# Kernel tuning notes

Hardware: AMD Instinct MI355X
Metric: run time of the kernel (lower is better)

The kernel has to match this reference:

```python
import jax, jax.numpy as jnp
import numpy as np

HIDDEN = 2048
N_HEADS = 32
N_KV_HEADS = 8
HEAD_DIM = HIDDEN // N_HEADS  # 64
N_REP = N_HEADS // N_KV_HEADS  # 4
ROPE_THETA = 10000.0


def setup_inputs() -> dict:
    key = jax.random.key(0)
    ks = jax.random.split(key, 5)
    b, s = 2, 2048
    x = jax.random.normal(ks[0], (b, s, HIDDEN), dtype=jnp.float32)
    position_ids = jnp.arange(b * s, dtype=jnp.int32).reshape(b, s)
    sc = 1.0 / np.sqrt(HIDDEN)
    Wq = jax.random.normal(ks[1], (HIDDEN, HIDDEN), dtype=jnp.float32) * sc
    Wk = jax.random.normal(ks[2], (HIDDEN, N_KV_HEADS * HEAD_DIM), dtype=jnp.float32) * sc
    Wv = jax.random.normal(ks[3], (HIDDEN, N_KV_HEADS * HEAD_DIM), dtype=jnp.float32) * sc
    Wo = jax.random.normal(ks[4], (HIDDEN, HIDDEN), dtype=jnp.float32) * sc
    return {"input_ids": x, "Wq": Wq, "Wk": Wk, "Wv": Wv, "Wo": Wo,
            "position_ids": position_ids}


def _rope_cos_sin(position_ids, dtype):
    # inv_freq: [head_dim/2]
    inv_freq = 1.0 / (ROPE_THETA ** (jnp.arange(0, HEAD_DIM, 2, dtype=jnp.float32) / HEAD_DIM))
    freqs = position_ids.astype(jnp.float32)[..., None] * inv_freq  # [b, s, d/2]
    emb = jnp.concatenate([freqs, freqs], axis=-1)  # [b, s, d]
    return emb.astype(dtype), None  # placeholder, replaced below


def _rotate_half(x):
    x1, x2 = jnp.split(x, 2, axis=-1)
    return jnp.concatenate([-x2, x1], axis=-1)


def reference(input_ids, Wq, Wk, Wv, Wo, position_ids):
    b, s, _ = input_ids.shape
    q = (input_ids @ Wq).reshape(b, s, N_HEADS, HEAD_DIM).transpose(0, 2, 1, 3)      # [b,H,s,d]
    k = (input_ids @ Wk).reshape(b, s, N_KV_HEADS, HEAD_DIM).transpose(0, 2, 1, 3)   # [b,Hkv,s,d]
    v = (input_ids @ Wv).reshape(b, s, N_KV_HEADS, HEAD_DIM).transpose(0, 2, 1, 3)

    # RoPE
    inv_freq = 1.0 / (ROPE_THETA ** (jnp.arange(0, HEAD_DIM, 2, dtype=jnp.float32) / HEAD_DIM))
    freqs = position_ids.astype(jnp.float32)[..., None] * inv_freq  # [b,s,d/2]
    emb = jnp.concatenate([freqs, freqs], axis=-1)                   # [b,s,d]
    cos = jnp.cos(emb).astype(input_ids.dtype)[:, None, :, :]        # [b,1,s,d]
    sin = jnp.sin(emb).astype(input_ids.dtype)[:, None, :, :]
    q = q * cos + _rotate_half(q) * sin
    k = k * cos + _rotate_half(k) * sin

    # repeat_kv: [b,Hkv,s,d] -> [b,H,s,d]
    k = jnp.repeat(k, N_REP, axis=1)
    v = jnp.repeat(v, N_REP, axis=1)

    # causal SDPA
    scale = 1.0 / np.sqrt(HEAD_DIM)
    scores = jnp.einsum('bhqd,bhkd->bhqk', q, k) * scale
    causal = jnp.tril(jnp.ones((s, s), dtype=bool))
    scores = jnp.where(causal, scores, jnp.finfo(scores.dtype).min)
    attn = jax.nn.softmax(scores, axis=-1)
    out = jnp.einsum('bhqk,bhkd->bhqd', attn, v)                     # [b,H,s,d]
    out = out.transpose(0, 2, 1, 3).reshape(b, s, HIDDEN)
    return out @ Wo
```

## Files before the change

kernel.cpp:

```cpp
#include <hip/hip_runtime.h>
#include <hip/hip_bf16.h>

#define HIDDEN 2048
#define NHEADS 32
#define NKVH   8
#define HD     64
#define BATCH  2
#define SEQ    2048
#define ROWS   (BATCH * SEQ)
#define NQKV   3072
#define KCOL   2048
#define VCOL   2560

typedef __bf16 bf16x8 __attribute__((ext_vector_type(8)));
typedef __bf16 bf16x4 __attribute__((ext_vector_type(4)));
typedef float  f32x4  __attribute__((ext_vector_type(4)));
typedef short  s16x4  __attribute__((ext_vector_type(4)));
typedef short  s16x8  __attribute__((ext_vector_type(8)));

__device__ __forceinline__ void gl2lds16(const void* g, void* l) {
  __builtin_amdgcn_global_load_lds(
      (const __attribute__((address_space(1))) void*)g,
      (__attribute__((address_space(3))) void*)l, 16, 0, 0);
}

__device__ __forceinline__ short f2bs(float f) {
  __bf16 h = (__bf16)f;
  return __builtin_bit_cast(short, h);
}

__device__ __forceinline__ float fexp2(float x) {
#if __has_builtin(__builtin_amdgcn_exp2f)
  return __builtin_amdgcn_exp2f(x);
#else
  return exp2f(x);
#endif
}

__device__ __forceinline__ f32x4 mfma16(s16x4 a, s16x4 b, f32x4 c) {
#if __has_builtin(__builtin_amdgcn_mfma_f32_16x16x16bf16_1k)
  return __builtin_amdgcn_mfma_f32_16x16x16bf16_1k(a, b, c, 0, 0, 0);
#else
  s16x8 a8 = __builtin_shufflevector(a, (s16x4){0,0,0,0}, 0,1,2,3,4,5,6,7);
  s16x8 b8 = __builtin_shufflevector(b, (s16x4){0,0,0,0}, 0,1,2,3,4,5,6,7);
  a8[4]=0;a8[5]=0;a8[6]=0;a8[7]=0; b8[4]=0;b8[5]=0;b8[6]=0;b8[7]=0;
  return __builtin_amdgcn_mfma_f32_16x16x32_bf16(
      __builtin_bit_cast(bf16x8, a8), __builtin_bit_cast(bf16x8, b8), c, 0, 0, 0);
#endif
}

__global__ void prep(const float* __restrict__ Wq, const float* __restrict__ Wk,
                     const float* __restrict__ Wv, const float* __restrict__ Wo,
                     const float* __restrict__ x,
                     __bf16* __restrict__ dstW, __bf16* __restrict__ Xb) {
  __shared__ __bf16 tile[32][33];
  int bid = blockIdx.x, tid = threadIdx.x;
  if (bid < 10240) {
    int n0 = (bid % 160) * 32, k0 = (bid / 160) * 32;
    int tx = tid & 31, ty = tid >> 5;
    const float* src;
    int N, c0;
    if (n0 < 2048)      { src = Wq; N = 2048; c0 = n0; }
    else if (n0 < 2560) { src = Wk; N = 512;  c0 = n0 - 2048; }
    else if (n0 < 3072) { src = Wv; N = 512;  c0 = n0 - 2560; }
    else                { src = Wo; N = 2048; c0 = n0 - 3072; }
#pragma unroll
    for (int i = 0; i < 32; i += 8)
      tile[ty + i][tx] = (__bf16)src[(size_t)(k0 + ty + i) * N + (c0 + tx)];
    __syncthreads();
#pragma unroll
    for (int i = 0; i < 32; i += 8)
      dstW[(size_t)(n0 + ty + i) * HIDDEN + (k0 + tx)] = tile[tx][ty + i];
  } else {
    size_t i = (size_t)(bid - 10240) * 256 + tid;
    const float4* s = (const float4*)(x + i * 16);
    float4 a = s[0], b = s[1], c = s[2], d = s[3];
    bf16x8 o0, o1;
    o0[0] = (__bf16)a.x; o0[1] = (__bf16)a.y; o0[2] = (__bf16)a.z; o0[3] = (__bf16)a.w;
    o0[4] = (__bf16)b.x; o0[5] = (__bf16)b.y; o0[6] = (__bf16)b.z; o0[7] = (__bf16)b.w;
    o1[0] = (__bf16)c.x; o1[1] = (__bf16)c.y; o1[2] = (__bf16)c.z; o1[3] = (__bf16)c.w;
    o1[4] = (__bf16)d.x; o1[5] = (__bf16)d.y; o1[6] = (__bf16)d.z; o1[7] = (__bf16)d.w;
    *(bf16x8*)(Xb + i * 16)     = o0;
    *(bf16x8*)(Xb + i * 16 + 8) = o1;
  }
}

template <typename OutT, bool ROPE>
__launch_bounds__(256, 2)
__global__ void gemm_bt(const __bf16* __restrict__ A, const __bf16* __restrict__ Bt,
                        OutT* __restrict__ C, int M, int N, int K,
                        const int* __restrict__ pos_ids, __bf16* __restrict__ Vt) {
  __shared__ __bf16 As[2][128 * 32];
  __shared__ __bf16 Bs[2][128 * 32];
  int id = blockIdx.x;
  int bm = (id & 7) * 4 + ((id >> 3) & 3);
  int bn = id >> 5;
  int t = threadIdx.x;
  int wave = t >> 6, lane = t & 63, l16 = lane & 15, quad = lane >> 4;
  int wm = (wave >> 1) * 64, wn = (wave & 1) * 64;

  f32x4 acc[4][4] = {};

  int arow = t >> 2;
  int ac   = (t & 3) * 8;
  const __bf16* Ag = A  + (size_t)(bm * 128 + arow) * K + ac;
  const __bf16* Bg = Bt + (size_t)(bn * 128 + arow) * K + ac;
  int woff = wave * 512;

  for (int k0 = 0; k0 < K; k0 += 64) {
    __syncthreads();
    gl2lds16(Ag + k0,                      &As[0][woff]);
    gl2lds16(Ag + (size_t)64 * K + k0,      &As[0][2048 + woff]);
    gl2lds16(Ag + k0 + 32,                 &As[1][woff]);
    gl2lds16(Ag + (size_t)64 * K + k0 + 32, &As[1][2048 + woff]);
    gl2lds16(Bg + k0,                      &Bs[0][woff]);
    gl2lds16(Bg + (size_t)64 * K + k0,      &Bs[0][2048 + woff]);
    gl2lds16(Bg + k0 + 32,                 &Bs[1][woff]);
    gl2lds16(Bg + (size_t)64 * K + k0 + 32, &Bs[1][2048 + woff]);
    __syncthreads();

#pragma unroll
    for (int ks = 0; ks < 2; ++ks) {
      bf16x8 af[4], bfr[4];
#pragma unroll
      for (int i = 0; i < 4; ++i) {
        af[i]  = *(const bf16x8*)(&As[ks][(wm + i * 16 + l16) * 32 + quad * 8]);
        bfr[i] = *(const bf16x8*)(&Bs[ks][(wn + i * 16 + l16) * 32 + quad * 8]);
      }
#pragma unroll
      for (int i = 0; i < 4; ++i)
#pragma unroll
        for (int j = 0; j < 4; ++j)
          acc[i][j] = __builtin_amdgcn_mfma_f32_16x16x32_bf16(af[i], bfr[j], acc[i][j], 0, 0, 0);
    }
  }

  if (ROPE) {
    int headidx = bn * 2 + (wn >> 6);
    if (headidx >= 40) {
#pragma unroll
      for (int i = 0; i < 4; ++i) {
        int srow = bm * 128 + wm + i * 16 + quad * 4;
        int b = srow >> 11, s = srow & 2047;
#pragma unroll
        for (int j = 0; j < 4; ++j) {
          int vcol = bn * 128 + wn + j * 16 + l16 - VCOL;
          int hk = vcol >> 6, d = vcol & 63;
          bf16x4 w;
#pragma unroll
          for (int r = 0; r < 4; ++r) w[r] = (__bf16)acc[i][j][r];
          *(bf16x4*)(Vt + ((size_t)(b * NKVH + hk) * HD + d) * SEQ + s) = w;
        }
      }
      return;
    }
    float invrev0 = __expf(-(float)l16 * 0.28782313662425574f) * 0.15915494309189535f;
    float invrev1 = __expf(-(float)(l16 + 16) * 0.28782313662425574f) * 0.15915494309189535f;
#pragma unroll
    for (int i = 0; i < 4; ++i)
#pragma unroll
      for (int r = 0; r < 4; ++r) {
        int gr = bm * 128 + wm + i * 16 + quad * 4 + r;
        float pos = (float)pos_ids[gr];
        float rv0 = pos * invrev0; rv0 -= floorf(rv0);
        float rv1 = pos * invrev1; rv1 -= floorf(rv1);
        float a0 = rv0 * 6.283185307179586f, a1 = rv1 * 6.283185307179586f;
        float s0 = __sinf(a0), c0 = __cosf(a0);
        float s1 = __sinf(a1), c1 = __cosf(a1);
        float x0 = acc[i][0][r], x2 = acc[i][2][r];
        acc[i][0][r] = x0 * c0 - x2 * s0;
        acc[i][2][r] = x2 * c0 + x0 * s0;
        float x1 = acc[i][1][r], x3 = acc[i][3][r];
        acc[i][1][r] = x1 * c1 - x3 * s1;
        acc[i][3][r] = x3 * c1 + x1 * s1;
      }
  }

#pragma unroll
  for (int i = 0; i < 4; ++i)
#pragma unroll
    for (int j = 0; j < 4; ++j)
#pragma unroll
      for (int r = 0; r < 4; ++r)
        C[(size_t)(bm * 128 + wm + i * 16 + quad * 4 + r) * N +
          (bn * 128 + wn + j * 16 + l16)] = (OutT)acc[i][j][r];
}

__launch_bounds__(256, 4)
__global__ void flash_attn(const __bf16* __restrict__ QKV, const __bf16* __restrict__ Vt,
                           __bf16* __restrict__ O) {
  int wgid = blockIdx.x + 64 * (blockIdx.y + 8 * (int)blockIdx.z);
  int swz  = (wgid & 7) * 128 + (wgid >> 3);
  int b  = swz >> 9;
  int hk = (swz >> 6) & 7;
  int bx = swz & 63;
  int p  = bx >> 2;
  int h  = hk * 4 + (bx & 3);

  int t = threadIdx.x;
  int wave = t >> 6, lane = t & 63, l16 = lane & 15, quad = lane >> 4;

  __shared__ __bf16 Ks[2][2][64 * 32];
  __shared__ __bf16 Vs[2][4096];

  const __bf16* Kbase = QKV + (size_t)(b * SEQ) * NQKV + KCOL + hk * HD;
  const __bf16* VtB   = Vt + (size_t)(b * NKVH + hk) * HD * SEQ;

  int kr = wave * 16 + (lane >> 2);
  int kc = (lane & 3) * 8;
  int vd = wave * 16 + (lane >> 2);
  int vsc = (lane & 3) * 16;
  int vs4w = (lane & 3) * 4;

  const s16x4 vones = { (short)0x3F80, (short)0x3F80, (short)0x3F80, (short)0x3F80 };

  for (int seg = 0; seg < 2; ++seg) {
    int qt = seg ? (31 - p) : p;

    __syncthreads();

    bf16x8 qfrag[2];
    {
      const __bf16* qp = QKV + (size_t)(b * SEQ + qt * 64 + wave * 16 + l16) * NQKV
                       + h * HD + quad * 8;
      bf16x8 q0 = *(const bf16x8*)qp;
      bf16x8 q1 = *(const bf16x8*)(qp + 32);
#pragma unroll
      for (int e = 0; e < 8; ++e) {
        qfrag[0][e] = (__bf16)((float)q0[e] * 0.18033688011112042f);
        qfrag[1][e] = (__bf16)((float)q1[e] * 0.18033688011112042f);
      }
    }

    f32x4 lacc = {0.f, 0.f, 0.f, 0.f};
    f32x4 oacc[4];
#pragma unroll
    for (int dt = 0; dt < 4; ++dt) oacc[dt] = (f32x4){0.f, 0.f, 0.f, 0.f};

    {
      const __bf16* kp = Kbase + (size_t)kr * NQKV + kc;
      gl2lds16(kp,      &Ks[0][0][wave * 512]);
      gl2lds16(kp + 32, &Ks[0][1][wave * 512]);
      const __bf16* vp = VtB + (size_t)vd * SEQ + vsc;
      s16x8 v0 = __builtin_bit_cast(s16x8, *(const bf16x8*)vp);
      s16x8 v1 = __builtin_bit_cast(s16x8, *(const bf16x8*)(vp + 8));
      *(s16x4*)(&Vs[0][(vs4w + 0) * 256 + vd * 4]) = __builtin_shufflevector(v0, v0, 0, 1, 2, 3);
      *(s16x4*)(&Vs[0][(vs4w + 1) * 256 + vd * 4]) = __builtin_shufflevector(v0, v0, 4, 5, 6, 7);
      *(s16x4*)(&Vs[0][(vs4w + 2) * 256 + vd * 4]) = __builtin_shufflevector(v1, v1, 0, 1, 2, 3);
      *(s16x4*)(&Vs[0][(vs4w + 3) * 256 + vd * 4]) = __builtin_shufflevector(v1, v1, 4, 5, 6, 7);
    }

    for (int kt = 0; kt <= qt; ++kt) {
      int buf = kt & 1;
      __syncthreads();

      bool pre = (kt < qt);
      s16x8 pv0, pv1;
      if (pre) {
        const __bf16* kp = Kbase + (size_t)((kt + 1) * 64 + kr) * NQKV + kc;
        gl2lds16(kp,      &Ks[buf ^ 1][0][wave * 512]);
        gl2lds16(kp + 32, &Ks[buf ^ 1][1][wave * 512]);
        const __bf16* vp = VtB + (size_t)vd * SEQ + (kt + 1) * 64 + vsc;
        pv0 = __builtin_bit_cast(s16x8, *(const bf16x8*)vp);
        pv1 = __builtin_bit_cast(s16x8, *(const bf16x8*)(vp + 8));
      }

      f32x4 sacc[4];
#pragma unroll
      for (int nt = 0; nt < 4; ++nt) sacc[nt] = (f32x4){0.f, 0.f, 0.f, 0.f};
#pragma unroll
      for (int ks = 0; ks < 2; ++ks) {
        bf16x8 kf[4];
#pragma unroll
        for (int nt = 0; nt < 4; ++nt)
          kf[nt] = *(const bf16x8*)(&Ks[buf][ks][(nt * 16 + l16) * 32 + quad * 8]);
#pragma unroll
        for (int nt = 0; nt < 4; ++nt)
          sacc[nt] = __builtin_amdgcn_mfma_f32_16x16x32_bf16(kf[nt], qfrag[ks], sacc[nt], 0, 0, 0);
      }

      s16x4 af[4];
      if (kt == qt) {
        int qg = wave * 16 + l16;
#pragma unroll
        for (int nt = 0; nt < 4; ++nt)
#pragma unroll
          for (int r = 0; r < 4; ++r) {
            int kg = nt * 16 + quad * 4 + r;
            float e = fexp2((kg > qg) ? -1e30f : sacc[nt][r]);
            af[nt][r] = f2bs(e);
          }
      } else {
#pragma unroll
        for (int nt = 0; nt < 4; ++nt)
#pragma unroll
          for (int r = 0; r < 4; ++r)
            af[nt][r] = f2bs(fexp2(sacc[nt][r]));
      }

#pragma unroll
      for (int nt = 0; nt < 4; ++nt) {
        s16x4 vf[4];
#pragma unroll
        for (int dt = 0; dt < 4; ++dt)
          vf[dt] = *(const s16x4*)(&Vs[buf][(nt * 4 + quad) * 256 + (dt * 16 + l16) * 4]);
#pragma unroll
        for (int dt = 0; dt < 4; ++dt)
          oacc[dt] = mfma16(af[nt], vf[dt], oacc[dt]);
        lacc = mfma16(af[nt], vones, lacc);
      }

      if (pre) {
        *(s16x4*)(&Vs[buf ^ 1][(vs4w + 0) * 256 + vd * 4]) = __builtin_shufflevector(pv0, pv0, 0, 1, 2, 3);
        *(s16x4*)(&Vs[buf ^ 1][(vs4w + 1) * 256 + vd * 4]) = __builtin_shufflevector(pv0, pv0, 4, 5, 6, 7);
        *(s16x4*)(&Vs[buf ^ 1][(vs4w + 2) * 256 + vd * 4]) = __builtin_shufflevector(pv1, pv1, 0, 1, 2, 3);
        *(s16x4*)(&Vs[buf ^ 1][(vs4w + 3) * 256 + vd * 4]) = __builtin_shufflevector(pv1, pv1, 4, 5, 6, 7);
      }
    }

#pragma unroll
    for (int r = 0; r < 4; ++r) {
      float inv = 1.0f / lacc[r];
#pragma unroll
      for (int dt = 0; dt < 4; ++dt) {
        float o = oacc[dt][r] * inv;
        O[(size_t)(b * SEQ + qt * 64 + wave * 16 + quad * 4 + r) * HIDDEN +
          h * HD + dt * 16 + l16] = (__bf16)o;
      }
    }
  }
}

extern "C" void kernel_launch(void* const* d_in, const int* in_sizes, int n_in,
                              void* d_out, int out_size, void* d_ws, size_t ws_size,
                              hipStream_t stream) {
  const float* x  = (const float*)d_in[0];
  const float* Wq = (const float*)d_in[1];
  const float* Wk = (const float*)d_in[2];
  const float* Wv = (const float*)d_in[3];
  const float* Wo = (const float*)d_in[4];
  const int* pos  = (const int*)d_in[5];

  __bf16* Wqkvt = (__bf16*)d_ws;
  __bf16* Wot   = Wqkvt + (size_t)NQKV * HIDDEN;
  __bf16* Xb    = Wot + (size_t)HIDDEN * HIDDEN;
  __bf16* QKV   = Xb + (size_t)ROWS * HIDDEN;
  __bf16* Oat   = QKV + (size_t)ROWS * NQKV;
  __bf16* Vt    = Xb;

  prep<<<dim3(12288), 256, 0, stream>>>(Wq, Wk, Wv, Wo, x, Wqkvt, Xb);

  gemm_bt<__bf16, true><<<dim3(768), 256, 0, stream>>>(
      Xb, Wqkvt, QKV, ROWS, NQKV, HIDDEN, pos, Vt);

  flash_attn<<<dim3(64, NKVH, BATCH), 256, 0, stream>>>(QKV, Vt, Oat);

  gemm_bt<float, false><<<dim3(512), 256, 0, stream>>>(
      Oat, Wot, (float*)d_out, ROWS, HIDDEN, HIDDEN, nullptr, nullptr);
}
```

Before: 276.8 us.

## Process both causal query tiles in one KV pass to share K/V loads

Each workgroup used to handle two query tiles (p and 31-p) one after another, streaming K/V from global memory separately for each. Now it holds both Q tiles in registers and makes a single pass over the KV tiles up to 31-p, applying each loaded K/V tile to both queries while kt <= p. This removes the duplicated K/V loads and barriers of the shorter pass, and s_setprio hints are added around the MFMA groups. The cost is more accumulator registers, which may lower occupancy under the 256x4 launch bounds, and divergent branch code for the a0 predicate.

After: 285.9 us. 3.3% more time.

```diff
diff --git a/kernel.cpp b/kernel.cpp
--- a/kernel.cpp
+++ b/kernel.cpp
@@ -195,6 +195,7 @@
   int hk = (swz >> 6) & 7;
   int bx = swz & 63;
   int p  = bx >> 2;
+  int np = 31 - p;
   int h  = hk * 4 + (bx & 3);
 
   int t = threadIdx.x;
@@ -214,116 +215,156 @@
 
   const s16x4 vones = { (short)0x3F80, (short)0x3F80, (short)0x3F80, (short)0x3F80 };
 
-  for (int seg = 0; seg < 2; ++seg) {
-    int qt = seg ? (31 - p) : p;
-
+  bf16x8 qfrag[2][2];
+#pragma unroll
+  for (int qi = 0; qi < 2; ++qi) {
+    int qt = qi ? np : p;
+    const __bf16* qp = QKV + (size_t)(b * SEQ + qt * 64 + wave * 16 + l16) * NQKV
+                     + h * HD + quad * 8;
+    bf16x8 q0 = *(const bf16x8*)qp;
+    bf16x8 q1 = *(const bf16x8*)(qp + 32);
+#pragma unroll
+    for (int e = 0; e < 8; ++e) {
+      qfrag[qi][0][e] = (__bf16)((float)q0[e] * 0.18033688011112042f);
+      qfrag[qi][1][e] = (__bf16)((float)q1[e] * 0.18033688011112042f);
+    }
+  }
+
+  f32x4 lacc[2] = { {0.f,0.f,0.f,0.f}, {0.f,0.f,0.f,0.f} };
+  f32x4 oacc[2][4];
+#pragma unroll
+  for (int qi = 0; qi < 2; ++qi)
+#pragma unroll
+    for (int dt = 0; dt < 4; ++dt) oacc[qi][dt] = (f32x4){0.f, 0.f, 0.f, 0.f};
+
+  {
+    const __bf16* kp = Kbase + (size_t)kr * NQKV + kc;
+    gl2lds16(kp,      &Ks[0][0][wave * 512]);
+    gl2lds16(kp + 32, &Ks[0][1][wave * 512]);
+    const __bf16* vp = VtB + (size_t)vd * SEQ + vsc;
+    s16x8 v0 = __builtin_bit_cast(s16x8, *(const bf16x8*)vp);
+    s16x8 v1 = __builtin_bit_cast(s16x8, *(const bf16x8*)(vp + 8));
+    *(s16x4*)(&Vs[0][(vs4w + 0) * 256 + vd * 4]) = __builtin_shufflevector(v0, v0, 0, 1, 2, 3);
+    *(s16x4*)(&Vs[0][(vs4w + 1) * 256 + vd * 4]) = __builtin_shufflevector(v0, v0, 4, 5, 6, 7);
+    *(s16x4*)(&Vs[0][(vs4w + 2) * 256 + vd * 4]) = __builtin_shufflevector(v1, v1, 0, 1, 2, 3);
+    *(s16x4*)(&Vs[0][(vs4w + 3) * 256 + vd * 4]) = __builtin_shufflevector(v1, v1, 4, 5, 6, 7);
+  }
+
+  for (int kt = 0; kt <= np; ++kt) {
+    int buf = kt & 1;
     __syncthreads();
 
-    bf16x8 qfrag[2];
+    bool pre = (kt < np);
+    s16x8 pv0, pv1;
+    if (pre) {
+      const __bf16* kp = Kbase + (size_t)((kt + 1) * 64 + kr) * NQKV + kc;
+      gl2lds16(kp,      &Ks[buf ^ 1][0][wave * 512]);
+      gl2lds16(kp + 32, &Ks[buf ^ 1][1][wave * 512]);
+      const __bf16* vp = VtB + (size_t)vd * SEQ + (kt + 1) * 64 + vsc;
+      pv0 = __builtin_bit_cast(s16x8, *(const bf16x8*)vp);
+      pv1 = __builtin_bit_cast(s16x8, *(const bf16x8*)(vp + 8));
+    }
+
+    bool a0 = (kt <= p);
+
+    f32x4 s0[4], s1[4];
+#pragma unroll
+    for (int nt = 0; nt < 4; ++nt) {
+      s0[nt] = (f32x4){0.f, 0.f, 0.f, 0.f};
+      s1[nt] = (f32x4){0.f, 0.f, 0.f, 0.f};
+    }
+#pragma unroll
+    for (int ks = 0; ks < 2; ++ks) {
+      bf16x8 kf[4];
+#pragma unroll
+      for (int nt = 0; nt < 4; ++nt)
+        kf[nt] = *(const bf16x8*)(&Ks[buf][ks][(nt * 16 + l16) * 32 + quad * 8]);
+      __builtin_amdgcn_s_setprio(1);
+#pragma unroll
+      for (int nt = 0; nt < 4; ++nt)
+        s1[nt] = __builtin_amdgcn_mfma_f32_16x16x32_bf16(kf[nt], qfrag[1][ks], s1[nt], 0, 0, 0);
+      if (a0) {
+#pragma unroll
+        for (int nt = 0; nt < 4; ++nt)
+          s0[nt] = __builtin_amdgcn_mfma_f32_16x16x32_bf16(kf[nt], qfrag[0][ks], s0[nt], 0, 0, 0);
+      }
+      __builtin_amdgcn_s_setprio(0);
+    }
+
+    s16x4 af0[4], af1[4];
     {
-      const __bf16* qp = QKV + (size_t)(b * SEQ + qt * 64 + wave * 16 + l16) * NQKV
-                       + h * HD + quad * 8;
-      bf16x8 q0 = *(const bf16x8*)qp;
-      bf16x8 q1 = *(const bf16x8*)(qp + 32);
-#pragma unroll
-      for (int e = 0; e < 8; ++e) {
-        qfrag[0][e] = (__bf16)((float)q0[e] * 0.18033688011112042f);
-        qfrag[1][e] = (__bf16)((float)q1[e] * 0.18033688011112042f);
-      }
-    }
-
-    f32x4 lacc = {0.f, 0.f, 0.f, 0.f};
-    f32x4 oacc[4];
-#pragma unroll
-    for (int dt = 0; dt < 4; ++dt) oacc[dt] = (f32x4){0.f, 0.f, 0.f, 0.f};
-
-    {
-      const __bf16* kp = Kbase + (size_t)kr * NQKV + kc;
-      gl2lds16(kp,      &Ks[0][0][wave * 512]);
-      gl2lds16(kp + 32, &Ks[0][1][wave * 512]);
-      const __bf16* vp = VtB + (size_t)vd * SEQ + vsc;
-      s16x8 v0 = __builtin_bit_cast(s16x8, *(const bf16x8*)vp);
-      s16x8 v1 = __builtin_bit_cast(s16x8, *(const bf16x8*)(vp + 8));
-      *(s16x4*)(&Vs[0][(vs4w + 0) * 256 + vd * 4]) = __builtin_shufflevector(v0, v0, 0, 1, 2, 3);
-      *(s16x4*)(&Vs[0][(vs4w + 1) * 256 + vd * 4]) = __builtin_shufflevector(v0, v0, 4, 5, 6, 7);
-      *(s16x4*)(&Vs[0][(vs4w + 2) * 256 + vd * 4]) = __builtin_shufflevector(v1, v1, 0, 1, 2, 3);
-      *(s16x4*)(&Vs[0][(vs4w + 3) * 256 + vd * 4]) = __builtin_shufflevector(v1, v1, 4, 5, 6, 7);
-    }
-
-    for (int kt = 0; kt <= qt; ++kt) {
-      int buf = kt & 1;
-      __syncthreads();
-
-      bool pre = (kt < qt);
-      s16x8 pv0, pv1;
-      if (pre) {
-        const __bf16* kp = Kbase + (size_t)((kt + 1) * 64 + kr) * NQKV + kc;
-        gl2lds16(kp,      &Ks[buf ^ 1][0][wave * 512]);
-        gl2lds16(kp + 32, &Ks[buf ^ 1][1][wave * 512]);
-        const __bf16* vp = VtB + (size_t)vd * SEQ + (kt + 1) * 64 + vsc;
-        pv0 = __builtin_bit_cast(s16x8, *(const bf16x8*)vp);
-        pv1 = __builtin_bit_cast(s16x8, *(const bf16x8*)(vp + 8));
-      }
-
-      f32x4 sacc[4];
-#pragma unroll
-      for (int nt = 0; nt < 4; ++nt) sacc[nt] = (f32x4){0.f, 0.f, 0.f, 0.f};
-#pragma unroll
-      for (int ks = 0; ks < 2; ++ks) {
-        bf16x8 kf[4];
-#pragma unroll
-        for (int nt = 0; nt < 4; ++nt)
-          kf[nt] = *(const bf16x8*)(&Ks[buf][ks][(nt * 16 + l16) * 32 + quad * 8]);
-#pragma unroll
-        for (int nt = 0; nt < 4; ++nt)
-          sacc[nt] = __builtin_amdgcn_mfma_f32_16x16x32_bf16(kf[nt], qfrag[ks], sacc[nt], 0, 0, 0);
-      }
-
-      s16x4 af[4];
-      if (kt == qt) {
-        int qg = wave * 16 + l16;
+      int qg = wave * 16 + l16;
+      if (kt == np) {
 #pragma unroll
         for (int nt = 0; nt < 4; ++nt)
 #pragma unroll
           for (int r = 0; r < 4; ++r) {
             int kg = nt * 16 + quad * 4 + r;
-            float e = fexp2((kg > qg) ? -1e30f : sacc[nt][r]);
-            af[nt][r] = f2bs(e);
+            af1[nt][r] = f2bs(fexp2((kg > qg) ? -1e30f : s1[nt][r]));
           }
       } else {
 #pragma unroll
         for (int nt = 0; nt < 4; ++nt)
 #pragma unroll
           for (int r = 0; r < 4; ++r)
-            af[nt][r] = f2bs(fexp2(sacc[nt][r]));
-      }
-
-#pragma unroll
-      for (int nt = 0; nt < 4; ++nt) {
-        s16x4 vf[4];
+            af1[nt][r] = f2bs(fexp2(s1[nt][r]));
+      }
+      if (a0) {
+        if (kt == p) {
+#pragma unroll
+          for (int nt = 0; nt < 4; ++nt)
+#pragma unroll
+            for (int r = 0; r < 4; ++r) {
+              int kg = nt * 16 + quad * 4 + r;
+              af0[nt][r] = f2bs(fexp2((kg > qg) ? -1e30f : s0[nt][r]));
+            }
+        } else {
+#pragma unroll
+          for (int nt = 0; nt < 4; ++nt)
+#pragma unroll
+            for (int r = 0; r < 4; ++r)
+              af0[nt][r] = f2bs(fexp2(s0[nt][r]));
+        }
+      }
+    }
+
+#pragma unroll
+    for (int nt = 0; nt < 4; ++nt) {
+      s16x4 vf[4];
+#pragma unroll
+      for (int dt = 0; dt < 4; ++dt)
+        vf[dt] = *(const s16x4*)(&Vs[buf][(nt * 4 + quad) * 256 + (dt * 16 + l16) * 4]);
+      __builtin_amdgcn_s_setprio(1);
+#pragma unroll
+      for (int dt = 0; dt < 4; ++dt)
+        oacc[1][dt] = mfma16(af1[nt], vf[dt], oacc[1][dt]);
+      lacc[1] = mfma16(af1[nt], vones, lacc[1]);
+      if (a0) {
 #pragma unroll
         for (int dt = 0; dt < 4; ++dt)
-          vf[dt] = *(const s16x4*)(&Vs[buf][(nt * 4 + quad) * 256 + (dt * 16 + l16) * 4]);
-#pragma unroll
-        for (int dt = 0; dt < 4; ++dt)
-          oacc[dt] = mfma16(af[nt], vf[dt], oacc[dt]);
-        lacc = mfma16(af[nt], vones, lacc);
-      }
-
-      if (pre) {
-        *(s16x4*)(&Vs[buf ^ 1][(vs4w + 0) * 256 + vd * 4]) = __builtin_shufflevector(pv0, pv0, 0, 1, 2, 3);
-        *(s16x4*)(&Vs[buf ^ 1][(vs4w + 1) * 256 + vd * 4]) = __builtin_shufflevector(pv0, pv0, 4, 5, 6, 7);
-        *(s16x4*)(&Vs[buf ^ 1][(vs4w + 2) * 256 + vd * 4]) = __builtin_shufflevector(pv1, pv1, 0, 1, 2, 3);
-        *(s16x4*)(&Vs[buf ^ 1][(vs4w + 3) * 256 + vd * 4]) = __builtin_shufflevector(pv1, pv1, 4, 5, 6, 7);
-      }
-    }
-
+          oacc[0][dt] = mfma16(af0[nt], vf[dt], oacc[0][dt]);
+        lacc[0] = mfma16(af0[nt], vones, lacc[0]);
+      }
+      __builtin_amdgcn_s_setprio(0);
+    }
+
+    if (pre) {
+      *(s16x4*)(&Vs[buf ^ 1][(vs4w + 0) * 256 + vd * 4]) = __builtin_shufflevector(pv0, pv0, 0, 1, 2, 3);
+      *(s16x4*)(&Vs[buf ^ 1][(vs4w + 1) * 256 + vd * 4]) = __builtin_shufflevector(pv0, pv0, 4, 5, 6, 7);
+      *(s16x4*)(&Vs[buf ^ 1][(vs4w + 2) * 256 + vd * 4]) = __builtin_shufflevector(pv1, pv1, 0, 1, 2, 3);
+      *(s16x4*)(&Vs[buf ^ 1][(vs4w + 3) * 256 + vd * 4]) = __builtin_shufflevector(pv1, pv1, 4, 5, 6, 7);
+    }
+  }
+
+#pragma unroll
+  for (int qi = 0; qi < 2; ++qi) {
+    int qt = qi ? np : p;
 #pragma unroll
     for (int r = 0; r < 4; ++r) {
-      float inv = 1.0f / lacc[r];
+      float inv = 1.0f / lacc[qi][r];
 #pragma unroll
       for (int dt = 0; dt < 4; ++dt) {
-        float o = oacc[dt][r] * inv;
+        float o = oacc[qi][dt][r] * inv;
         O[(size_t)(b * SEQ + qt * 64 + wave * 16 + quad * 4 + r) * HIDDEN +
           h * HD + dt * 16 + l16] = (__bf16)o;
       }
```
